# Performance work log

Measured on AMD Instinct MI355X. Metric: run time of the kernel, lower is better.

The kernel has to match this reference:

```python
import jax, jax.numpy as jnp
import numpy as np

N_HEADS = 8
HEAD_DIM = 32
GROUPS = 32
EPS = 1e-5


def setup_inputs() -> dict:
    key = jax.random.key(0)
    ks = jax.random.split(key, 3)
    b, c, h, w = 8, 256, 32, 32
    x = jax.random.normal(ks[0], (b, c, h, w), dtype=jnp.float32)
    norm_w = jnp.ones((c,), dtype=jnp.float32)
    norm_b = jnp.zeros((c,), dtype=jnp.float32)
    qkv_w = jax.random.normal(ks[1], (3 * c, c), dtype=jnp.float32) * (c ** -0.5)
    qkv_b = jnp.zeros((3 * c,), dtype=jnp.float32)
    out_w = jax.random.normal(ks[2], (c, c), dtype=jnp.float32) * (c ** -0.5)
    out_b = jnp.zeros((c,), dtype=jnp.float32)
    return {"x": x, "norm_w": norm_w, "norm_b": norm_b,
            "qkv_w": qkv_w, "qkv_b": qkv_b, "out_w": out_w, "out_b": out_b}


def _group_norm(x, weight, bias):
    b, c, h, w = x.shape
    xr = x.reshape(b, GROUPS, -1)  # [b, 32, (c//32)*h*w]
    mu = xr.mean(axis=-1, keepdims=True)
    var = xr.var(axis=-1, keepdims=True)
    xn = ((xr - mu) * jax.lax.rsqrt(var + EPS)).reshape(b, c, h, w)
    return xn * weight[:, None, None] + bias[:, None, None]


def _conv1x1(x, w, b):
    # 1x1 conv == channel matmul
    return jnp.einsum('oc,bchw->bohw', w, x) + b[None, :, None, None]


def reference(x, norm_w, norm_b, qkv_w, qkv_b, out_w, out_b):
    b, c, h, w = x.shape
    hw = h * w
    scale = HEAD_DIM ** (-0.5)
    qkv = _conv1x1(_group_norm(x, norm_w, norm_b), qkv_w, qkv_b)  # [b, 3c, h, w]
    q, k, v = jnp.split(qkv, 3, axis=1)
    # torch reshape(b, n_heads, c//n_heads, h*w) is a raw row-major reshape
    q = q.reshape(b, N_HEADS, HEAD_DIM, hw) * scale
    k = k.reshape(b, N_HEADS, HEAD_DIM, hw)
    v = v.reshape(b, N_HEADS, HEAD_DIM, hw)
    sim = jnp.einsum('bhdi,bhdj->bhij', q, k)  # [b, heads, hw, hw]
    sim = sim - jax.lax.stop_gradient(sim.max(axis=-1, keepdims=True))
    attn = jax.nn.softmax(sim, axis=-1)
    out = jnp.einsum('bhij,bhdj->bhid', attn, v)  # [b, heads, hw, head_dim]
    # faithful to the original: raw reshape (b, heads, hw, head_dim) -> (b, c, h, w)
    out = out.reshape(b, c, h, w)
    return _conv1x1(out, out_w, out_b) + x
```

## Files before the change

### kernel.cpp

```cpp
#include <hip/hip_runtime.h>
#include <hip/hip_bf16.h>

#define NB 8
#define NC 256
#define NHW 1024

typedef unsigned short u16;
typedef unsigned int u32;
using f16x8  = __attribute__((ext_vector_type(8))) _Float16;
using f32x16 = __attribute__((ext_vector_type(16))) float;
using u32x4  = __attribute__((ext_vector_type(4))) unsigned int;
using u16x8  = __attribute__((ext_vector_type(8))) unsigned short;

static __device__ inline u16 f2h(float f) {
    _Float16 h = (_Float16)f;
    return __builtin_bit_cast(u16, h);
}
static __device__ inline float h2f(u16 u) {
    return (float)__builtin_bit_cast(_Float16, u);
}
static __device__ inline unsigned pk2(float a, float b) {
    auto r = __builtin_amdgcn_cvt_pkrtz(a, b);
    return __builtin_bit_cast(unsigned, r);
}
static __device__ inline float vmax16(const f32x16& v) {
    float m0 = fmaxf(fmaxf(v[0], v[1]), fmaxf(v[2], v[3]));
    float m1 = fmaxf(fmaxf(v[4], v[5]), fmaxf(v[6], v[7]));
    float m2 = fmaxf(fmaxf(v[8], v[9]), fmaxf(v[10], v[11]));
    float m3 = fmaxf(fmaxf(v[12], v[13]), fmaxf(v[14], v[15]));
    return fmaxf(fmaxf(m0, m1), fmaxf(m2, m3));
}
static __device__ inline float vsum16(const f32x16& v) {
    float s0 = (v[0] + v[1]) + (v[2] + v[3]);
    float s1 = (v[4] + v[5]) + (v[6] + v[7]);
    float s2 = (v[8] + v[9]) + (v[10] + v[11]);
    float s3 = (v[12] + v[13]) + (v[14] + v[15]);
    return (s0 + s1) + (s2 + s3);
}
template<int B>
static __device__ inline f16x8 packP(const f32x16& p, const int h) {
    unsigned u0 = pk2(p[B + 0], p[B + 1]);
    unsigned u1 = pk2(p[B + 2], p[B + 3]);
    unsigned u2 = pk2(p[B + 4], p[B + 5]);
    unsigned u3 = pk2(p[B + 6], p[B + 7]);
    unsigned pu0 = __shfl_xor(u0, 32);
    unsigned pu1 = __shfl_xor(u1, 32);
    unsigned pu2 = __shfl_xor(u2, 32);
    unsigned pu3 = __shfl_xor(u3, 32);
    u32x4 w;
    w[0] = h ? pu2 : u0;
    w[1] = h ? pu3 : u1;
    w[2] = h ? u2 : pu0;
    w[3] = h ? u3 : pu1;
    return __builtin_bit_cast(f16x8, w);
}

#define QSCALE 0.25505412f

__global__ __launch_bounds__(256) void prep_kernel(
    const float* __restrict__ x, const float* __restrict__ qkv_w,
    const float* __restrict__ out_w, float2* __restrict__ stats,
    u16* __restrict__ Wq, u16* __restrict__ Wo)
{
    __shared__ float rs[4][2];
    const int bid = blockIdx.x, t = threadIdx.x;
    if (bid < 256) {
        const int g = bid & 31, b = bid >> 5;
        const size_t base = ((size_t)b * NC + g * 8) * NHW;
        const float4* xi = (const float4*)(x + base);
        float sum = 0.f, sq = 0.f;
#pragma unroll
        for (int i = 0; i < 8; ++i) {
            float4 v = xi[t + i * 256];
            sum += v.x + v.y + v.z + v.w;
            sq += v.x * v.x + v.y * v.y + v.z * v.z + v.w * v.w;
        }
        const int lane = t & 63, wv = t >> 6;
#pragma unroll
        for (int o = 32; o > 0; o >>= 1) {
            sum += __shfl_down(sum, o, 64);
            sq += __shfl_down(sq, o, 64);
        }
        if (lane == 0) { rs[wv][0] = sum; rs[wv][1] = sq; }
        __syncthreads();
        if (t == 0) {
            float S = rs[0][0] + rs[1][0] + rs[2][0] + rs[3][0];
            float Q = rs[0][1] + rs[1][1] + rs[2][1] + rs[3][1];
            float mu = S * (1.f / 8192.f);
            float var = Q * (1.f / 8192.f) - mu * mu;
            stats[b * 32 + g] = make_float2(mu, rsqrtf(var + 1e-5f));
        }
    } else {
        const int f4 = (bid - 256) * 256 + t;
        float4 v;
        u16* dhp;
        int e;
        if (f4 < 49152) {
            e = f4 * 4;
            v = *(const float4*)&qkv_w[e];
            if ((e >> 8) < 256) {
                v.x *= QSCALE; v.y *= QSCALE; v.z *= QSCALE; v.w *= QSCALE;
            }
            dhp = Wq;
        } else {
            e = (f4 - 49152) * 4;
            v = *(const float4*)&out_w[e];
            dhp = Wo;
        }
        ushort4 hh;
        hh.x = f2h(v.x); hh.y = f2h(v.y); hh.z = f2h(v.z); hh.w = f2h(v.w);
        *(ushort4*)&dhp[e] = hh;
    }
}

__global__ __launch_bounds__(256) void qkv_gemm_kernel(
    const u16* __restrict__ W, const float* __restrict__ x,
    const float2* __restrict__ stats,
    const float* __restrict__ gw, const float* __restrict__ gb,
    const float* __restrict__ bias,
    u16* __restrict__ qT, u16* __restrict__ kT, u16* __restrict__ vN)
{
    __shared__ __align__(16) u16 sB[2][2048];
    const int b = blockIdx.z;
    const int m0 = blockIdx.y * 128, n0 = blockIdx.x * 64;
    const int t = threadIdx.x, w = t >> 6, lane = t & 63;
    const int l31 = lane & 31, h = lane >> 5;
    const int msub = m0 + w * 32;

    const u16* War = W + (size_t)(msub + l31) * 256 + h * 8;

    const float bscale = (msub < 256) ? QSCALE : 1.0f;
    f32x16 acc[2];
#pragma unroll
    for (int r = 0; r < 16; ++r) {
        const int crow = (r & 3) + 8 * (r >> 2) + 4 * h;
        const float bv = bias[msub + crow] * bscale;
        acc[0][r] = bv; acc[1][r] = bv;
    }

    const int sn = t & 63;
    const int sw = w;
    const float* xs = x + (size_t)b * 256 * 1024 + (size_t)(sw * 8) * 1024 + n0 + sn;
    float vreg[8];
    const int woff = sn * 32 + ((sw ^ ((sn >> 1) & 3)) * 8);

#define LOADX(kcn) { _Pragma("unroll") for (int j = 0; j < 8; ++j) \
        vreg[j] = xs[(size_t)((kcn) * 32 + j) * 1024]; }
#define STAGE(kcn, buf) { \
        const int cb = (kcn) * 32 + sw * 8; \
        const float2 st = stats[b * 32 + (cb >> 3)]; \
        u32x4 pkv; \
        _Pragma("unroll") for (int jp = 0; jp < 4; ++jp) { \
            const float sc0 = gw[cb + jp * 2] * st.y; \
            const float of0 = gb[cb + jp * 2] - st.x * sc0; \
            const float sc1 = gw[cb + jp * 2 + 1] * st.y; \
            const float of1 = gb[cb + jp * 2 + 1] - st.x * sc1; \
            pkv[jp] = pk2(vreg[jp * 2] * sc0 + of0, vreg[jp * 2 + 1] * sc1 + of1); } \
        *(u32x4*)&sB[buf][woff] = pkv; }

    LOADX(0);
    STAGE(0, 0);
    __syncthreads();
    int cur = 0;
    for (int kc = 0; kc < 8; ++kc) {
        if (kc < 7) LOADX(kc + 1);
#pragma unroll
        for (int k16 = 0; k16 < 2; ++k16) {
            const f16x8 ah = *(const f16x8*)(War + kc * 32 + k16 * 16);
#pragma unroll
            for (int ns = 0; ns < 2; ++ns) {
                const int row = ns * 32 + l31;
                const int gi = ((k16 * 2 + h) ^ ((row >> 1) & 3)) * 8;
                const f16x8 bh = *(const f16x8*)&sB[cur][row * 32 + gi];
                acc[ns] = __builtin_amdgcn_mfma_f32_32x32x16_f16(ah, bh, acc[ns], 0, 0, 0);
            }
        }
        if (kc < 7) STAGE(kc + 1, cur ^ 1);
        __syncthreads();
        cur ^= 1;
    }
#undef LOADX
#undef STAGE

    const int type = msub >> 8;
    const int head = (msub >> 5) & 7;
    const int bh_ = b * 8 + head;
    if (type < 2) {
        u16* dst = type ? kT : qT;
#pragma unroll
        for (int ns = 0; ns < 2; ++ns) {
            const int n = n0 + ns * 32 + l31;
            u16* p = dst + ((size_t)bh_ * 1024 + n) * 32;
#pragma unroll
            for (int rp = 0; rp < 8; ++rp) {
                const int r = rp * 2;
                const int d = (r & 3) + 8 * (r >> 2) + 4 * h;
                *(unsigned*)&p[d] = (unsigned)f2h(acc[ns][r]) | ((unsigned)f2h(acc[ns][r + 1]) << 16);
            }
        }
    } else {
#pragma unroll
        for (int ns = 0; ns < 2; ++ns) {
            const int n = n0 + ns * 32 + l31;
#pragma unroll
            for (int r = 0; r < 16; ++r) {
                const int d = (r & 3) + 8 * (r >> 2) + 4 * h;
                vN[((size_t)bh_ * 32 + d) * 1024 + n] = f2h(acc[ns][r]);
            }
        }
    }
}

__global__ __launch_bounds__(256) void attn_mfma_kernel(
    const u16* __restrict__ qT, const u16* __restrict__ kT,
    const u16* __restrict__ vN, u16* __restrict__ ao)
{
    const int bid = blockIdx.x;
    const int itile = bid >> 6, bh = bid & 63;
    const int b = bh >> 3, head = bh & 7;
    const int t = threadIdx.x;
    const int lane = t & 63;
    const int w = t >> 6;
    const int l31 = lane & 31;
    const int h = lane >> 5;
    const int ibase = itile * 128 + w * 32;

    const u16* qrow = qT + ((size_t)bh * 1024 + ibase + l31) * 32;
    const f16x8 qf0 = *(const f16x8*)(qrow + h * 8);
    const f16x8 qf1 = *(const f16x8*)(qrow + 16 + h * 8);

    f32x16 out = {};
    float m = -1e30f, lsum = 0.f;

    const u16* kb = kT + (size_t)bh * 32768 + (size_t)l31 * 32 + h * 8;
    const u16* vb = vN + (size_t)bh * 32768 + (size_t)l31 * 1024 + h * 8;

    f16x8 ck0, ck1, ck2, ck3, cv0, cv1, cv2, cv3;
    f16x8 nk0, nk1, nk2, nk3, nv0, nv1, nv2, nv3;

#define LOADT(T, K0, K1, K2, K3, V0, V1, V2, V3) { \
    const u16* kp = kb + (T) * 2048; \
    K0 = *(const f16x8*)(kp); \
    K1 = *(const f16x8*)(kp + 16); \
    K2 = *(const f16x8*)(kp + 1024); \
    K3 = *(const f16x8*)(kp + 1024 + 16); \
    const u16* vp = vb + (T) * 64; \
    V0 = *(const f16x8*)(vp); \
    V1 = *(const f16x8*)(vp + 16); \
    V2 = *(const f16x8*)(vp + 32); \
    V3 = *(const f16x8*)(vp + 48); }

#define STEP(K0, K1, K2, K3, V0, V1, V2, V3) { \
    f32x16 sA = {}, sB = {}; \
    sA = __builtin_amdgcn_mfma_f32_32x32x16_f16(K0, qf0, sA, 0, 0, 0); \
    sA = __builtin_amdgcn_mfma_f32_32x32x16_f16(K1, qf1, sA, 0, 0, 0); \
    sB = __builtin_amdgcn_mfma_f32_32x32x16_f16(K2, qf0, sB, 0, 0, 0); \
    sB = __builtin_amdgcn_mfma_f32_32x32x16_f16(K3, qf1, sB, 0, 0, 0); \
    float mt = fmaxf(vmax16(sA), vmax16(sB)); \
    mt = fmaxf(mt, __shfl_xor(mt, 32)); \
    if (!__all(mt <= m + 8.f)) { \
        const float mn = fmaxf(m, mt); \
        const float cor = exp2f(m - mn); \
        m = mn; \
        lsum *= cor; \
        _Pragma("unroll") for (int r = 0; r < 16; ++r) { \
            const int src = (r & 3) + 8 * (r >> 2) + 4 * h; \
            out[r] *= __shfl(cor, src); \
        } \
    } \
    _Pragma("unroll") for (int r = 0; r < 16; ++r) { \
        sA[r] = exp2f(sA[r] - m); \
        sB[r] = exp2f(sB[r] - m); \
    } \
    float ps = vsum16(sA) + vsum16(sB); \
    ps += __shfl_xor(ps, 32); \
    lsum += ps; \
    const f16x8 pf0 = packP<0>(sA, h); \
    const f16x8 pf1 = packP<8>(sA, h); \
    const f16x8 pf2 = packP<0>(sB, h); \
    const f16x8 pf3 = packP<8>(sB, h); \
    out = __builtin_amdgcn_mfma_f32_32x32x16_f16(pf0, V0, out, 0, 0, 0); \
    out = __builtin_amdgcn_mfma_f32_32x32x16_f16(pf1, V1, out, 0, 0, 0); \
    out = __builtin_amdgcn_mfma_f32_32x32x16_f16(pf2, V2, out, 0, 0, 0); \
    out = __builtin_amdgcn_mfma_f32_32x32x16_f16(pf3, V3, out, 0, 0, 0); }

    LOADT(0, ck0, ck1, ck2, ck3, cv0, cv1, cv2, cv3);
    for (int T2 = 0; T2 < 8; ++T2) {
        LOADT(2 * T2 + 1, nk0, nk1, nk2, nk3, nv0, nv1, nv2, nv3);
        STEP(ck0, ck1, ck2, ck3, cv0, cv1, cv2, cv3);
        if (T2 < 7) {
            LOADT(2 * T2 + 2, ck0, ck1, ck2, ck3, cv0, cv1, cv2, cv3);
        }
        STEP(nk0, nk1, nk2, nk3, nv0, nv1, nv2, nv3);
    }
#undef LOADT
#undef STEP

    const float linv = 1.f / lsum;
    const int cOut = b * 256 + head * 32 + itile * 4 + w;
    u16* og = ao + (size_t)cOut * 1024 + l31;
#pragma unroll
    for (int r = 0; r < 16; ++r) {
        const int crow = (r & 3) + 8 * (r >> 2) + 4 * h;
        const float sc = __shfl(linv, crow);
        og[crow * 32] = f2h(out[r] * sc);
    }
}

__global__ __launch_bounds__(256) void out_gemm_kernel(
    const u16* __restrict__ W, const u16* __restrict__ ao,
    const float* __restrict__ bias,
    const float* __restrict__ res, float* __restrict__ Y)
{
    __shared__ __align__(16) u16 sB[2][2048];
    const int b = blockIdx.z;
    const int m0 = blockIdx.y * 64, n0 = blockIdx.x * 64;
    const int t = threadIdx.x, w = t >> 6, lane = t & 63;
    const int l31 = lane & 31, h = lane >> 5;
    const int wm = w >> 1, wn = w & 1;
    const int msub = m0 + wm * 32;

    const u16* War = W + (size_t)(msub + l31) * 256 + h * 8;

    f32x16 acc;
#pragma unroll
    for (int r = 0; r < 16; ++r) {
        const int crow = (r & 3) + 8 * (r >> 2) + 4 * h;
        acc[r] = bias[msub + crow];
    }

    const int kL = t >> 3, pb = (t & 7) * 8;
    const u16* asrc = ao + ((size_t)b * 256 + kL) * 1024 + n0 + pb;
    u16x8 regs;

#define LOADC(kc) { regs = *(const u16x8*)(asrc + (size_t)(kc) * 32 * 1024); }
#define WRITEC(buf) { _Pragma("unroll") for (int e = 0; e < 8; ++e) { \
        const int n = pb + e; \
        const int idx = n * 32 + ((kL >> 3) ^ (n & 3)) * 8 + (kL & 7); \
        sB[buf][idx] = regs[e]; } }

    LOADC(0); WRITEC(0);
    __syncthreads();
    int cur = 0;
    for (int kc = 0; kc < 8; ++kc) {
        if (kc < 7) LOADC(kc + 1);
#pragma unroll
        for (int k16 = 0; k16 < 2; ++k16) {
            const f16x8 ah = *(const f16x8*)(War + kc * 32 + k16 * 16);
            const int gi = ((k16 * 2 + h) ^ (l31 & 3)) * 8;
            const int row = wn * 32 + l31;
            const f16x8 bh = *(const f16x8*)&sB[cur][row * 32 + gi];
            acc = __builtin_amdgcn_mfma_f32_32x32x16_f16(ah, bh, acc, 0, 0, 0);
        }
        if (kc < 7) WRITEC(cur ^ 1);
        __syncthreads();
        cur ^= 1;
    }
    const int n = n0 + wn * 32 + l31;
#pragma unroll
    for (int r = 0; r < 16; ++r) {
        const int mm = msub + (r & 3) + 8 * (r >> 2) + 4 * h;
        const size_t idx = ((size_t)b * 256 + mm) * 1024 + n;
        Y[idx] = acc[r] + res[idx];
    }
#undef LOADC
#undef WRITEC
}

extern "C" void kernel_launch(void* const* d_in, const int* in_sizes, int n_in,
                              void* d_out, int out_size, void* d_ws, size_t ws_size,
                              hipStream_t stream) {
    const float* x      = (const float*)d_in[0];
    const float* norm_w = (const float*)d_in[1];
    const float* norm_b = (const float*)d_in[2];
    const float* qkv_w  = (const float*)d_in[3];
    const float* qkv_b  = (const float*)d_in[4];
    const float* out_w  = (const float*)d_in[5];
    const float* out_b  = (const float*)d_in[6];
    float* out = (float*)d_out;

    char* p = (char*)d_ws;
    float2* stats = (float2*)p;  p += 4096;
    u16* Wq  = (u16*)p;  p += 393216 * 2;
    u16* Wo  = (u16*)p;  p += 131072 * 2;
    u16* qT  = (u16*)p;  p += 4u * 1024 * 1024;
    u16* kT  = (u16*)p;  p += 4u * 1024 * 1024;
    u16* vN  = (u16*)p;  p += 4u * 1024 * 1024;
    u16* ao  = (u16*)p;  p += 4u * 1024 * 1024;

    prep_kernel<<<512, 256, 0, stream>>>(x, qkv_w, out_w, stats, Wq, Wo);
    qkv_gemm_kernel<<<dim3(16, 6, NB), 256, 0, stream>>>(Wq, x, stats, norm_w, norm_b, qkv_b, qT, kT, vN);
    attn_mfma_kernel<<<512, 256, 0, stream>>>(qT, kT, vN, ao);
    out_gemm_kernel<<<dim3(16, 4, NB), 256, 0, stream>>>(Wo, ao, out_b, x, out);
}
```

Baseline: 68.37 us.

## Split attention over key halves and merge partial softmax results

Attention blocks now each process half of the key/value sequence, doubling the grid from 512 to 1024 blocks. Each block writes its unnormalized fp32 partial output plus its running max and sum. A new merge kernel rescales and combines the two halves and writes the normalized fp16 result in the original layout. This targets low occupancy on a GPU with many compute units, at the cost of an extra launch and about 16 MB of extra fp32 traffic written and read back.

```diff
diff --git a/kernel.cpp b/kernel.cpp
--- a/kernel.cpp
+++ b/kernel.cpp
@@ -213,10 +213,13 @@
 
 __global__ __launch_bounds__(256) void attn_mfma_kernel(
     const u16* __restrict__ qT, const u16* __restrict__ kT,
-    const u16* __restrict__ vN, u16* __restrict__ ao)
+    const u16* __restrict__ vN, float* __restrict__ pout,
+    float2* __restrict__ pml)
 {
     const int bid = blockIdx.x;
-    const int itile = bid >> 6, bh = bid & 63;
+    const int jh = bid >> 9;
+    const int rem = bid & 511;
+    const int itile = rem >> 6, bh = rem & 63;
     const int b = bh >> 3, head = bh & 7;
     const int t = threadIdx.x;
     const int lane = t & 63;
@@ -284,27 +287,58 @@
     out = __builtin_amdgcn_mfma_f32_32x32x16_f16(pf2, V2, out, 0, 0, 0); \
     out = __builtin_amdgcn_mfma_f32_32x32x16_f16(pf3, V3, out, 0, 0, 0); }
 
-    LOADT(0, ck0, ck1, ck2, ck3, cv0, cv1, cv2, cv3);
-    for (int T2 = 0; T2 < 8; ++T2) {
-        LOADT(2 * T2 + 1, nk0, nk1, nk2, nk3, nv0, nv1, nv2, nv3);
+    const int T0 = jh * 8;
+    LOADT(T0, ck0, ck1, ck2, ck3, cv0, cv1, cv2, cv3);
+    for (int T2 = 0; T2 < 4; ++T2) {
+        LOADT(T0 + 2 * T2 + 1, nk0, nk1, nk2, nk3, nv0, nv1, nv2, nv3);
         STEP(ck0, ck1, ck2, ck3, cv0, cv1, cv2, cv3);
-        if (T2 < 7) {
-            LOADT(2 * T2 + 2, ck0, ck1, ck2, ck3, cv0, cv1, cv2, cv3);
+        if (T2 < 3) {
+            LOADT(T0 + 2 * T2 + 2, ck0, ck1, ck2, ck3, cv0, cv1, cv2, cv3);
         }
         STEP(nk0, nk1, nk2, nk3, nv0, nv1, nv2, nv3);
     }
 #undef LOADT
 #undef STEP
 
-    const float linv = 1.f / lsum;
-    const int cOut = b * 256 + head * 32 + itile * 4 + w;
-    u16* og = ao + (size_t)cOut * 1024 + l31;
+    const size_t pbase = (size_t)(jh * 64 + bh) * 1024 + ibase;
+    float* po = pout + pbase * 32 + l31;
 #pragma unroll
     for (int r = 0; r < 16; ++r) {
         const int crow = (r & 3) + 8 * (r >> 2) + 4 * h;
-        const float sc = __shfl(linv, crow);
-        og[crow * 32] = f2h(out[r] * sc);
-    }
+        po[crow * 32] = out[r];
+    }
+    if (h == 0) pml[pbase + l31] = make_float2(m, lsum);
+}
+
+__global__ __launch_bounds__(256) void merge_kernel(
+    const float* __restrict__ pout, const float2* __restrict__ pml,
+    u16* __restrict__ ao)
+{
+    const int bid = blockIdx.x;
+    const int bh = bid >> 3, iblk = bid & 7;
+    const int t = threadIdx.x;
+    const int il = t >> 1, dh = (t & 1) * 16;
+    const int i = iblk * 128 + il;
+    const int base = bh * 1024 + i;
+    const float2 ml1 = pml[base];
+    const float2 ml2 = pml[65536 + base];
+    const float M = fmaxf(ml1.x, ml2.x);
+    const float c1 = exp2f(ml1.x - M);
+    const float c2 = exp2f(ml2.x - M);
+    const float inv = 1.f / (ml1.y * c1 + ml2.y * c2);
+    const float* o1 = pout + (size_t)base * 32 + dh;
+    const float* o2 = pout + (size_t)(65536 + base) * 32 + dh;
+    const int c = (bh >> 3) * 256 + (bh & 7) * 32 + (i >> 5);
+    const int p = (i & 31) * 32 + dh;
+    u16* dst = ao + (size_t)c * 1024 + p;
+    u16x8 wa, wb;
+#pragma unroll
+    for (int e = 0; e < 8; ++e) {
+        wa[e] = f2h((o1[e] * c1 + o2[e] * c2) * inv);
+        wb[e] = f2h((o1[8 + e] * c1 + o2[8 + e] * c2) * inv);
+    }
+    *(u16x8*)dst = wa;
+    *(u16x8*)(dst + 8) = wb;
 }
 
 __global__ __launch_bounds__(256) void out_gemm_kernel(
@@ -387,9 +421,12 @@
     u16* kT  = (u16*)p;  p += 4u * 1024 * 1024;
     u16* vN  = (u16*)p;  p += 4u * 1024 * 1024;
     u16* ao  = (u16*)p;  p += 4u * 1024 * 1024;
+    float* pout = (float*)p;  p += 16u * 1024 * 1024;
+    float2* pml = (float2*)p; p += 1024 * 1024;
 
     prep_kernel<<<512, 256, 0, stream>>>(x, qkv_w, out_w, stats, Wq, Wo);
     qkv_gemm_kernel<<<dim3(16, 6, NB), 256, 0, stream>>>(Wq, x, stats, norm_w, norm_b, qkv_b, qT, kT, vN);
-    attn_mfma_kernel<<<512, 256, 0, stream>>>(qT, kT, vN, ao);
+    attn_mfma_kernel<<<1024, 256, 0, stream>>>(qT, kT, vN, pout, pml);
+    merge_kernel<<<512, 256, 0, stream>>>(pout, pml, ao);
     out_gemm_kernel<<<dim3(16, 4, NB), 256, 0, stream>>>(Wo, ao, out_b, x, out);
 }
```

After: 71.22 us. +4.2%, slower.
